# Optimization experiments

Measured on AMD Instinct MI355X. Metric: run time of the kernel, lower is better.

Reference implementation:

```python
import jax, jax.numpy as jnp
import numpy as np
from jax import lax

B, C, D, H, W = 2, 256, 16, 16, 16
Cq = C // 4


def _conv3d(x, w, b, pad):
    # x: [B,C,D,H,W], w: [O,I,kd,kh,kw]
    y = lax.conv_general_dilated(x, w, (1, 1, 1), pad,
                                 dimension_numbers=("NCDHW", "OIDHW", "NCDHW"))
    return y + b[None, :, None, None, None]


def _ln_ch(x, scale, bias, eps=1e-5):
    # LayerNorm over channel dim (torch normalizes last dim after permute)
    mu = jnp.mean(x, axis=1, keepdims=True)
    var = jnp.var(x, axis=1, keepdims=True)
    y = (x - mu) * lax.rsqrt(var + eps)
    return y * scale[None, :, None, None, None] + bias[None, :, None, None, None]


def setup_inputs() -> dict:
    key = jax.random.key(0)
    ks = jax.random.split(key, 16)
    s = 0.05
    inp = {
        "x": jax.random.normal(ks[0], (B, C, D, H, W), jnp.float32),
        "w1": jax.random.normal(ks[1], (Cq, Cq, 1, 1, 1), jnp.float32) * s,
        "b1": jax.random.normal(ks[2], (Cq,), jnp.float32) * s,
        "w2": jax.random.normal(ks[3], (Cq, Cq, 1, 1, 1), jnp.float32) * s,
        "b2": jax.random.normal(ks[4], (Cq,), jnp.float32) * s,
        "w3": jax.random.normal(ks[5], (Cq, Cq, 1, 1, 1), jnp.float32) * s,
        "b3": jax.random.normal(ks[6], (Cq,), jnp.float32) * s,
        "w4": jax.random.normal(ks[7], (Cq, Cq, 1, 1, 1), jnp.float32) * s,
        "b4": jax.random.normal(ks[8], (Cq,), jnp.float32) * s,
        "wq": jax.random.normal(ks[9], (C, C, 1, 3, 1), jnp.float32) * s,
        "bq": jax.random.normal(ks[10], (C,), jnp.float32) * s,
        "wk": jax.random.normal(ks[11], (C, C, 1, 1, 3), jnp.float32) * s,
        "bk": jax.random.normal(ks[12], (C,), jnp.float32) * s,
        "wv": jax.random.normal(ks[13], (C, C, 3, 1, 1), jnp.float32) * s,
        "bv": jax.random.normal(ks[14], (C,), jnp.float32) * s,
        "q_scale": jnp.ones((C,), jnp.float32),
        "q_bias": jnp.zeros((C,), jnp.float32),
        "k_scale": jnp.ones((C,), jnp.float32),
        "k_bias": jnp.zeros((C,), jnp.float32),
        "v_scale": jnp.ones((C,), jnp.float32),
        "v_bias": jnp.zeros((C,), jnp.float32),
        "gamma": jnp.ones((1,), jnp.float32) * 0.5,
    }
    return inp


def reference(x, w1, b1, w2, b2, w3, b3, w4, b4, wq, bq, wk, bk, wv, bv,
              q_scale, q_bias, k_scale, k_bias, v_scale, v_bias, gamma):
    b, c, d, h, w = x.shape
    n = d * h * w
    p0 = [(0, 0)] * 3
    # channel-split 1x1 convs + SiLU gating (dilation is a no-op for 1x1x1)
    s1 = _conv3d(x[:, 0 * Cq:1 * Cq], w1, b1, p0)
    s2 = _conv3d(x[:, 1 * Cq:2 * Cq], w2, b2, p0)
    s3 = _conv3d(x[:, 2 * Cq:3 * Cq], w3, b3, p0)
    s4 = _conv3d(x[:, 3 * Cq:4 * Cq], w4, b4, p0)
    silu = lambda t: t * jax.nn.sigmoid(t)
    xg = jnp.concatenate([silu(s1), silu(s2), silu(s3), silu(s4)], axis=1)
    # QKV projections with directional kernels + channel LayerNorm
    Q = _ln_ch(_conv3d(xg, wq, bq, [(0, 0), (1, 1), (0, 0)]), q_scale, q_bias)
    K = _ln_ch(_conv3d(xg, wk, bk, [(0, 0), (0, 0), (1, 1)]), k_scale, k_bias)
    V = _ln_ch(_conv3d(xg, wv, bv, [(1, 1), (0, 0), (0, 0)]), v_scale, v_bias)
    Qf = Q.reshape(b, c, n).transpose(0, 2, 1)  # [B, N, C]
    Kf = K.reshape(b, c, n).transpose(0, 2, 1)
    Vf = V.reshape(b, c, n).transpose(0, 2, 1)
    scores = jnp.einsum("bnc,bmc->bnm", Qf, Kf) / (c ** 0.5)  # [B, N, N]
    att = jax.nn.softmax(scores, axis=-1)
    out_a = jnp.einsum("bnm,bmc->bnc", att, Vf)  # [B, N, C]
    out_a = out_a.transpose(0, 2, 1).reshape(b, c, d, h, w)
    return gamma * out_a + xg
```

## Files before the change

kernel.cpp:

```cpp
#include <hip/hip_runtime.h>

#define Bn 2
#define Cn 256
#define Nn 4096
#define SPLIT 4
#define KVB 32

typedef __attribute__((ext_vector_type(8))) short short8;
typedef __attribute__((ext_vector_type(4))) float f32x4;

__device__ __forceinline__ unsigned short f2bf(float f) {
  union { float f; unsigned int u; } v; v.f = f;
  unsigned int r = (v.u + 0x7FFFu + ((v.u >> 16) & 1u)) >> 16;
  return (unsigned short)r;
}

__device__ __forceinline__ f32x4 mfma16(short8 a, short8 b, f32x4 c) {
  return __builtin_amdgcn_mfma_f32_16x16x32_bf16(a, b, c, 0, 0, 0);
}

__global__ void prep_w_kernel(const float* __restrict__ wq,
                              const float* __restrict__ wk,
                              const float* __restrict__ wv,
                              unsigned short* __restrict__ w2) {
  int idx = blockIdx.x * 256 + threadIdx.x;
  int tensor = idx / 196608;
  int rem = idx % 196608;
  int t  = rem >> 16;
  int co = (rem >> 8) & 255;
  int ci = rem & 255;
  const float* w = (tensor == 0) ? wq : (tensor == 1) ? wk : wv;
  w2[idx] = f2bf(w[(co * 256 + ci) * 3 + t]);
}

__global__ __launch_bounds__(256) void gated_kernel(
    const float* __restrict__ x,
    const float* __restrict__ w1, const float* __restrict__ b1,
    const float* __restrict__ w2, const float* __restrict__ b2,
    const float* __restrict__ w3, const float* __restrict__ b3,
    const float* __restrict__ w4, const float* __restrict__ b4,
    float* __restrict__ xg, unsigned short* __restrict__ xgT) {
  __shared__ float Wl[64][65];
  __shared__ float Xl[64][65];
  __shared__ unsigned short Yl[64][72];
  const int tid = threadIdx.x;
  const int n0 = blockIdx.x * 64;
  const int q  = blockIdx.y;
  const int b  = blockIdx.z;
  const float* wsel = (q == 0) ? w1 : (q == 1) ? w2 : (q == 2) ? w3 : w4;
  const float* bsel = (q == 0) ? b1 : (q == 1) ? b2 : (q == 2) ? b3 : b4;

  #pragma unroll
  for (int it = 0; it < 4; it++) {
    int i = (tid + it * 256) * 4;
    float4 v = *(const float4*)(wsel + i);
    int co = i >> 6, ci = i & 63;
    Wl[co][ci] = v.x; Wl[co][ci + 1] = v.y; Wl[co][ci + 2] = v.z; Wl[co][ci + 3] = v.w;
  }
  {
    int ci = tid >> 2, part = tid & 3;
    const float* src = x + ((size_t)(b * Cn + q * 64 + ci)) * Nn + n0 + part * 16;
    #pragma unroll
    for (int j = 0; j < 4; j++) {
      float4 v = ((const float4*)src)[j];
      float* dst = &Xl[ci][part * 16 + j * 4];
      dst[0] = v.x; dst[1] = v.y; dst[2] = v.z; dst[3] = v.w;
    }
  }
  __syncthreads();
  const int co = tid >> 2, npart = tid & 3;
  float acc[16];
  {
    float bias = bsel[co];
    #pragma unroll
    for (int j = 0; j < 16; j++) acc[j] = bias;
  }
  for (int ci = 0; ci < 64; ci++) {
    float wv_ = Wl[co][ci];
    const float* xr = &Xl[ci][npart * 16];
    #pragma unroll
    for (int j = 0; j < 16; j++) acc[j] += wv_ * xr[j];
  }
  float* xgp = xg + ((size_t)(b * Cn + q * 64 + co)) * Nn + n0 + npart * 16;
  #pragma unroll
  for (int j = 0; j < 16; j++) {
    float v = acc[j];
    float s = v / (1.f + __expf(-v));
    xgp[j] = s;
    Yl[npart * 16 + j][co] = f2bf(s);
  }
  __syncthreads();
  {
    int r = tid >> 2, cp = tid & 3;
    union { unsigned short u[16]; uint4 v[2]; } pk;
    #pragma unroll
    for (int j = 0; j < 16; j++) pk.u[j] = Yl[r][cp * 16 + j];
    uint4* dst = (uint4*)(xgT + ((size_t)(b * Nn + n0 + r)) * Cn + q * 64 + cp * 16);
    dst[0] = pk.v[0];
    dst[1] = pk.v[1];
  }
}

__global__ __launch_bounds__(256, 2) void qkvconv_kernel(
    const unsigned short* __restrict__ xgT, const unsigned short* __restrict__ w2,
    const float* __restrict__ bq, const float* __restrict__ bk,
    const float* __restrict__ bv, float* __restrict__ pre) {
  __shared__ unsigned short Al[64][40];
  __shared__ unsigned short Bl[64][40];
  const int tid = threadIdx.x;
  const int lane = tid & 63, wave = tid >> 6;
  const int l15 = lane & 15, l4 = lane >> 4;
  const int n0  = blockIdx.x * 64;
  const int co0 = blockIdx.y * 64;
  const int tensor = blockIdx.z >> 1;
  const int b = blockIdx.z & 1;
  const int cstride = (tensor == 0) ? 16 : (tensor == 1) ? 1 : 256;
  const float* bias = (tensor == 0) ? bq : (tensor == 1) ? bk : bv;
  const unsigned short* wbase = w2 + (size_t)tensor * 196608;
  const unsigned short* xbase = xgT + (size_t)b * Nn * Cn;

  f32x4 acc[4];
  #pragma unroll
  for (int i = 0; i < 4; i++) acc[i] = (f32x4){0.f, 0.f, 0.f, 0.f};

  const int arow = tid >> 2, akp = tid & 3;
  const int n = n0 + arow;
  const int coordv = (n / cstride) & 15;

  for (int kc = 0; kc < 24; kc++) {
    int t = kc >> 3;
    int cib = (kc & 7) * 32;
    int shift = t - 1;
    int c2 = coordv + shift;
    const unsigned short* asrc =
        xbase + ((size_t)(n + shift * cstride)) * Cn + cib + akp * 8;
    uint4 av = (c2 >= 0 && c2 < 16) ? *(const uint4*)asrc : (uint4){0, 0, 0, 0};
    *(uint4*)&Al[arow][akp * 8] = av;
    const unsigned short* bsrc =
        wbase + ((size_t)(t * 256 + co0 + arow)) * 256 + cib + akp * 8;
    *(uint4*)&Bl[arow][akp * 8] = *(const uint4*)bsrc;
    __syncthreads();
    short8 af = *(const short8*)&Al[wave * 16 + l15][l4 * 8];
    #pragma unroll
    for (int ct = 0; ct < 4; ct++) {
      short8 bf = *(const short8*)&Bl[ct * 16 + l15][l4 * 8];
      acc[ct] = mfma16(af, bf, acc[ct]);
    }
    __syncthreads();
  }
  float* obase = pre + ((size_t)(tensor * Bn + b)) * Nn * Cn;
  #pragma unroll
  for (int ct = 0; ct < 4; ct++) {
    int co = co0 + ct * 16 + l15;
    float bv_ = bias[co];
    #pragma unroll
    for (int i = 0; i < 4; i++) {
      int nn = n0 + wave * 16 + l4 * 4 + i;
      obase[(size_t)nn * Cn + co] = acc[ct][i] + bv_;
    }
  }
}

__global__ __launch_bounds__(256) void ln_kernel(
    const float* __restrict__ pre, unsigned short* __restrict__ qkv,
    const float* __restrict__ qs, const float* __restrict__ qb,
    const float* __restrict__ ks, const float* __restrict__ kb,
    const float* __restrict__ vs, const float* __restrict__ vb) {
  const int nidx = blockIdx.x;
  const int b = blockIdx.y;
  const int tensor = blockIdx.z;
  const int c = threadIdx.x;
  const float* sc = (tensor == 0) ? qs : (tensor == 1) ? ks : vs;
  const float* bi = (tensor == 0) ? qb : (tensor == 1) ? kb : vb;
  size_t base = ((size_t)(tensor * Bn + b) * Nn + nidx) * Cn;
  float v = pre[base + c];
  float s = v, s2 = v * v;
  #pragma unroll
  for (int m = 1; m < 64; m <<= 1) {
    s  += __shfl_xor(s, m);
    s2 += __shfl_xor(s2, m);
  }
  __shared__ float red[8];
  int wave = threadIdx.x >> 6, lane = threadIdx.x & 63;
  if (lane == 0) { red[wave] = s; red[4 + wave] = s2; }
  __syncthreads();
  s  = red[0] + red[1] + red[2] + red[3];
  s2 = red[4] + red[5] + red[6] + red[7];
  float mean = s * (1.f / 256.f);
  float var  = s2 * (1.f / 256.f) - mean * mean;
  float inv  = rsqrtf(var + 1e-5f);
  float y = (v - mean) * inv * sc[c] + bi[c];
  qkv[base + c] = f2bf(y);
}

__global__ __launch_bounds__(256, 2) void flash_kernel(
    const unsigned short* __restrict__ qkv, float* __restrict__ Opart,
    float* __restrict__ ml) {
  __shared__ unsigned short Ks[KVB][264];
  __shared__ unsigned short Vt[256][40];
  __shared__ unsigned short Pl[4][16][40];
  const int tid = threadIdx.x, lane = tid & 63, wave = tid >> 6;
  const int l15 = lane & 15, l4 = lane >> 4;
  const int qt = blockIdx.x, b = blockIdx.y, sp = blockIdx.z;
  const unsigned short* Q = qkv + (size_t)(0 * Bn + b) * Nn * Cn;
  const unsigned short* K = qkv + (size_t)(1 * Bn + b) * Nn * Cn;
  const unsigned short* V = qkv + (size_t)(2 * Bn + b) * Nn * Cn;
  const int q0 = qt * 64 + wave * 16;

  short8 qf[8];
  {
    const unsigned short* qp = Q + (size_t)(q0 + l15) * Cn + l4 * 8;
    #pragma unroll
    for (int kk = 0; kk < 8; kk++) qf[kk] = *(const short8*)(qp + kk * 32);
  }
  f32x4 acc_o[16];
  #pragma unroll
  for (int i = 0; i < 16; i++) acc_o[i] = (f32x4){0.f, 0.f, 0.f, 0.f};
  float m_r[4], l_r[4];
  #pragma unroll
  for (int i = 0; i < 4; i++) { m_r[i] = -1e30f; l_r[i] = 0.f; }

  const int kvbase = sp * (Nn / SPLIT);
  const float scl = 0.0625f;

  for (int step = 0; step < (Nn / SPLIT) / KVB; step++) {
    int kv0 = kvbase + step * KVB;
    {
      int r = tid >> 3, cp = tid & 7;
      const unsigned short* src = K + (size_t)(kv0 + r) * Cn + cp * 32;
      uint4* dst = (uint4*)&Ks[r][cp * 32];
      #pragma unroll
      for (int i = 0; i < 4; i++) dst[i] = ((const uint4*)src)[i];
    }
    {
      int rp = (tid & 15) * 2, ch = (tid >> 4) * 16;
      const unsigned short* s0p = V + (size_t)(kv0 + rp) * Cn + ch;
      const unsigned short* s1p = s0p + Cn;
      union { uint4 v[2]; unsigned short u[16]; } r0, r1;
      r0.v[0] = ((const uint4*)s0p)[0]; r0.v[1] = ((const uint4*)s0p)[1];
      r1.v[0] = ((const uint4*)s1p)[0]; r1.v[1] = ((const uint4*)s1p)[1];
      #pragma unroll
      for (int j = 0; j < 16; j++) {
        unsigned int pack = (unsigned int)r0.u[j] | ((unsigned int)r1.u[j] << 16);
        *(unsigned int*)&Vt[ch + j][rp] = pack;
      }
    }
    __syncthreads();

    f32x4 s0 = (f32x4){0.f, 0.f, 0.f, 0.f};
    f32x4 s1 = (f32x4){0.f, 0.f, 0.f, 0.f};
    #pragma unroll
    for (int kk = 0; kk < 8; kk++) {
      short8 b0 = *(const short8*)&Ks[l15][kk * 32 + l4 * 8];
      short8 b1 = *(const short8*)&Ks[16 + l15][kk * 32 + l4 * 8];
      s0 = mfma16(qf[kk], b0, s0);
      s1 = mfma16(qf[kk], b1, s1);
    }

    float p0[4], p1[4], al[4];
    #pragma unroll
    for (int i = 0; i < 4; i++) {
      float a0 = s0[i] * scl, a1 = s1[i] * scl;
      float mt = fmaxf(a0, a1);
      mt = fmaxf(mt, __shfl_xor(mt, 1));
      mt = fmaxf(mt, __shfl_xor(mt, 2));
      mt = fmaxf(mt, __shfl_xor(mt, 4));
      mt = fmaxf(mt, __shfl_xor(mt, 8));
      float mn = fmaxf(m_r[i], mt);
      float a = __expf(m_r[i] - mn);
      m_r[i] = mn; al[i] = a;
      p0[i] = __expf(a0 - mn);
      p1[i] = __expf(a1 - mn);
      float r = p0[i] + p1[i];
      r += __shfl_xor(r, 1); r += __shfl_xor(r, 2);
      r += __shfl_xor(r, 4); r += __shfl_xor(r, 8);
      l_r[i] = l_r[i] * a + r;
    }
    #pragma unroll
    for (int i = 0; i < 4; i++) {
      int row = l4 * 4 + i;
      Pl[wave][row][l15]      = f2bf(p0[i]);
      Pl[wave][row][16 + l15] = f2bf(p1[i]);
    }
    #pragma unroll
    for (int ct = 0; ct < 16; ct++)
      #pragma unroll
      for (int i = 0; i < 4; i++) acc_o[ct][i] *= al[i];

    short8 pf = *(const short8*)&Pl[wave][l15][l4 * 8];
    #pragma unroll
    for (int ct = 0; ct < 16; ct++) {
      short8 vf = *(const short8*)&Vt[ct * 16 + l15][l4 * 8];
      acc_o[ct] = mfma16(pf, vf, acc_o[ct]);
    }
    __syncthreads();
  }

  float* ob = Opart + ((size_t)(sp * Bn + b) * Nn) * Cn;
  #pragma unroll
  for (int ct = 0; ct < 16; ct++) {
    int c = ct * 16 + l15;
    #pragma unroll
    for (int i = 0; i < 4; i++) {
      int nn = q0 + l4 * 4 + i;
      ob[(size_t)nn * Cn + c] = acc_o[ct][i];
    }
  }
  if (l15 == 0) {
    #pragma unroll
    for (int i = 0; i < 4; i++) {
      int nn = q0 + l4 * 4 + i;
      size_t mb = (((size_t)sp * Bn + b) * Nn + nn) * 2;
      ml[mb]     = m_r[i];
      ml[mb + 1] = l_r[i];
    }
  }
}

__global__ __launch_bounds__(256) void combine_kernel(
    const float* __restrict__ Opart, const float* __restrict__ ml,
    const float* __restrict__ xg, const float* __restrict__ gamma,
    float* __restrict__ out) {
  __shared__ float T[256][17];
  const int tid = threadIdx.x;
  const int n0 = blockIdx.x * 16;
  const int b = blockIdx.y;
  const float g = gamma[0];
  for (int r = 0; r < 16; r++) {
    int n = n0 + r;
    float msp[SPLIT], lsp[SPLIT];
    float mm = -1e30f;
    #pragma unroll
    for (int s = 0; s < SPLIT; s++) {
      size_t mb = (((size_t)s * Bn + b) * Nn + n) * 2;
      msp[s] = ml[mb]; lsp[s] = ml[mb + 1];
      mm = fmaxf(mm, msp[s]);
    }
    float denom = 0.f, w[SPLIT];
    #pragma unroll
    for (int s = 0; s < SPLIT; s++) { w[s] = __expf(msp[s] - mm); denom += w[s] * lsp[s]; }
    float inv = 1.f / denom;
    float acc = 0.f;
    #pragma unroll
    for (int s = 0; s < SPLIT; s++)
      acc += w[s] * Opart[(((size_t)s * Bn + b) * Nn + n) * Cn + tid];
    T[tid][r] = acc * inv;
  }
  __syncthreads();
  const int c = tid;
  const float4* xg4 = (const float4*)(xg + ((size_t)(b * Cn + c)) * Nn + n0);
  float4* op = (float4*)(out + ((size_t)(b * Cn + c)) * Nn + n0);
  #pragma unroll
  for (int r4 = 0; r4 < 4; r4++) {
    float4 xv = xg4[r4];
    float4 vv;
    vv.x = g * T[c][r4 * 4 + 0] + xv.x;
    vv.y = g * T[c][r4 * 4 + 1] + xv.y;
    vv.z = g * T[c][r4 * 4 + 2] + xv.z;
    vv.w = g * T[c][r4 * 4 + 3] + xv.w;
    op[r4] = vv;
  }
}

extern "C" void kernel_launch(void* const* d_in, const int* in_sizes, int n_in,
                              void* d_out, int out_size, void* d_ws, size_t ws_size,
                              hipStream_t stream) {
  const float* x   = (const float*)d_in[0];
  const float* w1  = (const float*)d_in[1];
  const float* b1  = (const float*)d_in[2];
  const float* w2i = (const float*)d_in[3];
  const float* b2  = (const float*)d_in[4];
  const float* w3  = (const float*)d_in[5];
  const float* b3  = (const float*)d_in[6];
  const float* w4  = (const float*)d_in[7];
  const float* b4  = (const float*)d_in[8];
  const float* wq  = (const float*)d_in[9];
  const float* bq  = (const float*)d_in[10];
  const float* wk  = (const float*)d_in[11];
  const float* bk  = (const float*)d_in[12];
  const float* wv  = (const float*)d_in[13];
  const float* bv  = (const float*)d_in[14];
  const float* qs  = (const float*)d_in[15];
  const float* qb  = (const float*)d_in[16];
  const float* ks  = (const float*)d_in[17];
  const float* kb  = (const float*)d_in[18];
  const float* vs  = (const float*)d_in[19];
  const float* vb  = (const float*)d_in[20];
  const float* gamma = (const float*)d_in[21];
  float* out = (float*)d_out;

  char* ws = (char*)d_ws;
  float* xg            = (float*)(ws + 0);
  unsigned short* xgT  = (unsigned short*)(ws + 8388608);
  unsigned short* w2b  = (unsigned short*)(ws + 12582912);
  float* pre           = (float*)(ws + 13762560);
  unsigned short* qkv  = (unsigned short*)(ws + 38928384);
  float* Opart         = (float*)(ws + 51511296);
  float* ml            = (float*)(ws + 85065728);

  prep_w_kernel<<<dim3(2304), dim3(256), 0, stream>>>(wq, wk, wv, w2b);
  gated_kernel<<<dim3(64, 4, 2), dim3(256), 0, stream>>>(
      x, w1, b1, w2i, b2, w3, b3, w4, b4, xg, xgT);
  qkvconv_kernel<<<dim3(64, 4, 6), dim3(256), 0, stream>>>(
      xgT, w2b, bq, bk, bv, pre);
  ln_kernel<<<dim3(4096, 2, 3), dim3(256), 0, stream>>>(
      pre, qkv, qs, qb, ks, kb, vs, vb);
  flash_kernel<<<dim3(64, 2, SPLIT), dim3(256), 0, stream>>>(qkv, Opart, ml);
  combine_kernel<<<dim3(256, 2), dim3(256), 0, stream>>>(Opart, ml, xg, gamma, out);
}
```

Baseline: 179.4 us.

## Swizzle flash LDS, bf16 partials, wave-per-row LayerNorm, and double KV split

The LayerNorm kernel now handles one row per wave with float4 loads and no shared-memory reduction. The flash kernel drops padded LDS arrays in favour of XOR-swizzled layouts for K, V-transpose and P, which cuts LDS footprint so launch bounds can allow more resident blocks. KV split rises from 4 to 8 for more parallelism, and partial outputs are stored as bf16 to halve combine traffic. The workspace is reshuffled so the bf16 partial buffer aliases the now-dead pre-LN buffer. Storing partials in bf16 lowers accumulation precision.

```diff
diff --git a/kernel.cpp b/kernel.cpp
--- a/kernel.cpp
+++ b/kernel.cpp
@@ -3,7 +3,7 @@
 #define Bn 2
 #define Cn 256
 #define Nn 4096
-#define SPLIT 4
+#define SPLIT 8
 #define KVB 32
 
 typedef __attribute__((ext_vector_type(8))) short short8;
@@ -13,6 +13,9 @@
   union { float f; unsigned int u; } v; v.f = f;
   unsigned int r = (v.u + 0x7FFFu + ((v.u >> 16) & 1u)) >> 16;
   return (unsigned short)r;
+}
+__device__ __forceinline__ float bf2f(unsigned short u) {
+  union { unsigned int i; float f; } v; v.i = ((unsigned int)u) << 16; return v.f;
 }
 
 __device__ __forceinline__ f32x4 mfma16(short8 a, short8 b, f32x4 c) {
@@ -166,39 +169,41 @@
     const float* __restrict__ qs, const float* __restrict__ qb,
     const float* __restrict__ ks, const float* __restrict__ kb,
     const float* __restrict__ vs, const float* __restrict__ vb) {
-  const int nidx = blockIdx.x;
+  const int tensor = blockIdx.z;
   const int b = blockIdx.y;
-  const int tensor = blockIdx.z;
-  const int c = threadIdx.x;
+  const int wave = threadIdx.x >> 6, lane = threadIdx.x & 63;
+  const int nidx = blockIdx.x * 4 + wave;
   const float* sc = (tensor == 0) ? qs : (tensor == 1) ? ks : vs;
   const float* bi = (tensor == 0) ? qb : (tensor == 1) ? kb : vb;
   size_t base = ((size_t)(tensor * Bn + b) * Nn + nidx) * Cn;
-  float v = pre[base + c];
-  float s = v, s2 = v * v;
+  float4 v = *(const float4*)(pre + base + lane * 4);
+  float s  = v.x + v.y + v.z + v.w;
+  float s2 = v.x * v.x + v.y * v.y + v.z * v.z + v.w * v.w;
   #pragma unroll
   for (int m = 1; m < 64; m <<= 1) {
     s  += __shfl_xor(s, m);
     s2 += __shfl_xor(s2, m);
   }
-  __shared__ float red[8];
-  int wave = threadIdx.x >> 6, lane = threadIdx.x & 63;
-  if (lane == 0) { red[wave] = s; red[4 + wave] = s2; }
-  __syncthreads();
-  s  = red[0] + red[1] + red[2] + red[3];
-  s2 = red[4] + red[5] + red[6] + red[7];
   float mean = s * (1.f / 256.f);
   float var  = s2 * (1.f / 256.f) - mean * mean;
   float inv  = rsqrtf(var + 1e-5f);
-  float y = (v - mean) * inv * sc[c] + bi[c];
-  qkv[base + c] = f2bf(y);
-}
-
-__global__ __launch_bounds__(256, 2) void flash_kernel(
-    const unsigned short* __restrict__ qkv, float* __restrict__ Opart,
+  int c = lane * 4;
+  float4 scv = *(const float4*)(sc + c);
+  float4 biv = *(const float4*)(bi + c);
+  union { unsigned short u[4]; uint2 v2; } pk;
+  pk.u[0] = f2bf((v.x - mean) * inv * scv.x + biv.x);
+  pk.u[1] = f2bf((v.y - mean) * inv * scv.y + biv.y);
+  pk.u[2] = f2bf((v.z - mean) * inv * scv.z + biv.z);
+  pk.u[3] = f2bf((v.w - mean) * inv * scv.w + biv.w);
+  *(uint2*)(qkv + base + c) = pk.v2;
+}
+
+__global__ __launch_bounds__(256, 4) void flash_kernel(
+    const unsigned short* __restrict__ qkv, unsigned short* __restrict__ Opart,
     float* __restrict__ ml) {
-  __shared__ unsigned short Ks[KVB][264];
-  __shared__ unsigned short Vt[256][40];
-  __shared__ unsigned short Pl[4][16][40];
+  __shared__ unsigned short Ks[32 * 256];
+  __shared__ unsigned short Vt[256 * 32];
+  __shared__ unsigned short Pl[4 * 16 * 32];
   const int tid = threadIdx.x, lane = tid & 63, wave = tid >> 6;
   const int l15 = lane & 15, l4 = lane >> 4;
   const int qt = blockIdx.x, b = blockIdx.y, sp = blockIdx.z;
@@ -226,11 +231,14 @@
   for (int step = 0; step < (Nn / SPLIT) / KVB; step++) {
     int kv0 = kvbase + step * KVB;
     {
-      int r = tid >> 3, cp = tid & 7;
-      const unsigned short* src = K + (size_t)(kv0 + r) * Cn + cp * 32;
-      uint4* dst = (uint4*)&Ks[r][cp * 32];
+      int r = tid >> 3, cb = tid & 7, rx = r & 7;
+      const unsigned short* src = K + (size_t)(kv0 + r) * Cn;
+      unsigned short* dst = Ks + r * 256;
       #pragma unroll
-      for (int i = 0; i < 4; i++) dst[i] = ((const uint4*)src)[i];
+      for (int i = 0; i < 4; i++) {
+        int chunk = cb + 8 * i;
+        *(uint4*)(dst + ((chunk ^ rx) * 8)) = *(const uint4*)(src + chunk * 8);
+      }
     }
     {
       int rp = (tid & 15) * 2, ch = (tid >> 4) * 16;
@@ -239,22 +247,29 @@
       union { uint4 v[2]; unsigned short u[16]; } r0, r1;
       r0.v[0] = ((const uint4*)s0p)[0]; r0.v[1] = ((const uint4*)s0p)[1];
       r1.v[0] = ((const uint4*)s1p)[0]; r1.v[1] = ((const uint4*)s1p)[1];
+      int kc = rp >> 3, kw = rp & 7;
       #pragma unroll
       for (int j = 0; j < 16; j++) {
+        int c = ch + j;
         unsigned int pack = (unsigned int)r0.u[j] | ((unsigned int)r1.u[j] << 16);
-        *(unsigned int*)&Vt[ch + j][rp] = pack;
+        *(unsigned int*)(Vt + c * 32 + ((kc ^ ((c >> 1) & 3)) * 8) + kw) = pack;
       }
     }
     __syncthreads();
 
     f32x4 s0 = (f32x4){0.f, 0.f, 0.f, 0.f};
     f32x4 s1 = (f32x4){0.f, 0.f, 0.f, 0.f};
-    #pragma unroll
-    for (int kk = 0; kk < 8; kk++) {
-      short8 b0 = *(const short8*)&Ks[l15][kk * 32 + l4 * 8];
-      short8 b1 = *(const short8*)&Ks[16 + l15][kk * 32 + l4 * 8];
-      s0 = mfma16(qf[kk], b0, s0);
-      s1 = mfma16(qf[kk], b1, s1);
+    {
+      const int r0x = l15 & 7;
+      const int r1x = l15 & 7;
+      #pragma unroll
+      for (int kk = 0; kk < 8; kk++) {
+        int ch = kk * 4 + l4;
+        short8 b0 = *(const short8*)(Ks + l15 * 256 + ((ch ^ r0x) * 8));
+        short8 b1 = *(const short8*)(Ks + (16 + l15) * 256 + ((ch ^ r1x) * 8));
+        s0 = mfma16(qf[kk], b0, s0);
+        s1 = mfma16(qf[kk], b1, s1);
+      }
     }
 
     float p0[4], p1[4], al[4];
@@ -279,31 +294,35 @@
     #pragma unroll
     for (int i = 0; i < 4; i++) {
       int row = l4 * 4 + i;
-      Pl[wave][row][l15]      = f2bf(p0[i]);
-      Pl[wave][row][16 + l15] = f2bf(p1[i]);
+      unsigned short* pb = Pl + wave * 512 + row * 32;
+      int rs = (row >> 1) & 3;
+      pb[(((l15 >> 3) ^ rs) * 8) + (l15 & 7)]       = f2bf(p0[i]);
+      pb[(((2 + (l15 >> 3)) ^ rs) * 8) + (l15 & 7)] = f2bf(p1[i]);
     }
     #pragma unroll
     for (int ct = 0; ct < 16; ct++)
       #pragma unroll
       for (int i = 0; i < 4; i++) acc_o[ct][i] *= al[i];
 
-    short8 pf = *(const short8*)&Pl[wave][l15][l4 * 8];
+    short8 pf = *(const short8*)(Pl + wave * 512 + l15 * 32 +
+                                 ((l4 ^ ((l15 >> 1) & 3)) * 8));
     #pragma unroll
     for (int ct = 0; ct < 16; ct++) {
-      short8 vf = *(const short8*)&Vt[ct * 16 + l15][l4 * 8];
+      int c = ct * 16 + l15;
+      short8 vf = *(const short8*)(Vt + c * 32 + ((l4 ^ ((c >> 1) & 3)) * 8));
       acc_o[ct] = mfma16(pf, vf, acc_o[ct]);
     }
     __syncthreads();
   }
 
-  float* ob = Opart + ((size_t)(sp * Bn + b) * Nn) * Cn;
+  unsigned short* ob = Opart + ((size_t)(sp * Bn + b) * Nn) * Cn;
   #pragma unroll
   for (int ct = 0; ct < 16; ct++) {
     int c = ct * 16 + l15;
     #pragma unroll
     for (int i = 0; i < 4; i++) {
       int nn = q0 + l4 * 4 + i;
-      ob[(size_t)nn * Cn + c] = acc_o[ct][i];
+      ob[(size_t)nn * Cn + c] = f2bf(acc_o[ct][i]);
     }
   }
   if (l15 == 0) {
@@ -318,7 +337,7 @@
 }
 
 __global__ __launch_bounds__(256) void combine_kernel(
-    const float* __restrict__ Opart, const float* __restrict__ ml,
+    const unsigned short* __restrict__ Opart, const float* __restrict__ ml,
     const float* __restrict__ xg, const float* __restrict__ gamma,
     float* __restrict__ out) {
   __shared__ float T[256][17];
@@ -343,7 +362,7 @@
     float acc = 0.f;
     #pragma unroll
     for (int s = 0; s < SPLIT; s++)
-      acc += w[s] * Opart[(((size_t)s * Bn + b) * Nn + n) * Cn + tid];
+      acc += w[s] * bf2f(Opart[(((size_t)s * Bn + b) * Nn + n) * Cn + tid]);
     T[tid][r] = acc * inv;
   }
   __syncthreads();
@@ -393,17 +412,17 @@
   float* xg            = (float*)(ws + 0);
   unsigned short* xgT  = (unsigned short*)(ws + 8388608);
   unsigned short* w2b  = (unsigned short*)(ws + 12582912);
-  float* pre           = (float*)(ws + 13762560);
-  unsigned short* qkv  = (unsigned short*)(ws + 38928384);
-  float* Opart         = (float*)(ws + 51511296);
-  float* ml            = (float*)(ws + 85065728);
+  unsigned short* qkv  = (unsigned short*)(ws + 13762560);
+  float* pre           = (float*)(ws + 26345472);
+  unsigned short* Opart = (unsigned short*)(ws + 26345472);
+  float* ml            = (float*)(ws + 59899904);
 
   prep_w_kernel<<<dim3(2304), dim3(256), 0, stream>>>(wq, wk, wv, w2b);
   gated_kernel<<<dim3(64, 4, 2), dim3(256), 0, stream>>>(
       x, w1, b1, w2i, b2, w3, b3, w4, b4, xg, xgT);
   qkvconv_kernel<<<dim3(64, 4, 6), dim3(256), 0, stream>>>(
       xgT, w2b, bq, bk, bv, pre);
-  ln_kernel<<<dim3(4096, 2, 3), dim3(256), 0, stream>>>(
+  ln_kernel<<<dim3(1024, 2, 3), dim3(256), 0, stream>>>(
       pre, qkv, qs, qb, ks, kb, vs, vb);
   flash_kernel<<<dim3(64, 2, SPLIT), dim3(256), 0, stream>>>(qkv, Opart, ml);
   combine_kernel<<<dim3(256, 2), dim3(256), 0, stream>>>(Opart, ml, xg, gamma, out);
```

New measurement: 241.7 us. +34.7%, slower.
